# Optimization experiments

Measured on AMD Instinct MI355X. Metric: run time of the kernel, lower is better.

The kernel has to match this reference:

```python
import jax, jax.numpy as jnp
import numpy as np

B, C, H, K = 1024, 1000, 768, 128

def setup_inputs() -> dict:
    key = jax.random.key(0)
    k1, k2, k3, k4 = jax.random.split(key, 4)
    x = jax.random.normal(k1, (B, H), dtype=jnp.float32)
    y = jax.random.randint(k2, (B,), 0, C)
    class_weights = jax.random.normal(k3, (C, H, K), dtype=jnp.float32) * 0.1
    class_bias = jnp.zeros((C, H), dtype=jnp.float32)
    # torch.nn.Linear default init (uniform in +/- 1/sqrt(H))
    bound = 1.0 / np.sqrt(H)
    W_lin = jax.random.uniform(k4, (H, H), dtype=jnp.float32, minval=-bound, maxval=bound)
    b_lin = jnp.zeros((H,), dtype=jnp.float32)
    return {"x": x, "y": y, "class_weights": class_weights,
            "class_bias": class_bias, "W_lin": W_lin, "b_lin": b_lin}

def reference(x, y, class_weights, class_bias, W_lin, b_lin):
    # one-hot matmul gather == true indexed gather (same math)
    weights = class_weights[y]                # [B, H, K]
    neg_x = jax.nn.relu(-x)                   # [B, H]
    x1 = jnp.tanh(neg_x @ W_lin.T + b_lin)    # [B, H]
    # x1[B,1,H] @ weights[B,H,K] -> sum over singleton dim == [B, K]
    logits = jnp.einsum('bh,bhk->bk', x1, weights)
    return logits
```

## Files before the change

### kernel.cpp

```cpp
#include <hip/hip_runtime.h>
#include <hip/hip_bf16.h>
#include <cstddef>

#define B_SZ 1024
#define C_SZ 1000
#define H_SZ 768
#define K_SZ 128

typedef __attribute__((ext_vector_type(8))) short bf16x8;
typedef __attribute__((ext_vector_type(4))) float f32x4;

#define WS_NEGX_OFF 0
#define WS_W_OFF    1572864
#define WS_X1_OFF   4194304

__global__ __launch_bounds__(256) void convert_pack(
    const float* __restrict__ x, const float* __restrict__ W,
    ushort* __restrict__ negx, ushort* __restrict__ Wb)
{
    const int NX = B_SZ * H_SZ / 4;
    const int NW = H_SZ * H_SZ / 4;
    int i = blockIdx.x * 256 + threadIdx.x;
    if (i < NX) {
        float4 v = ((const float4*)x)[i];
        union { ushort u[4]; ushort4 v4; } o;
        o.u[0] = __bfloat16_as_ushort(__float2bfloat16(fmaxf(-v.x, 0.f)));
        o.u[1] = __bfloat16_as_ushort(__float2bfloat16(fmaxf(-v.y, 0.f)));
        o.u[2] = __bfloat16_as_ushort(__float2bfloat16(fmaxf(-v.z, 0.f)));
        o.u[3] = __bfloat16_as_ushort(__float2bfloat16(fmaxf(-v.w, 0.f)));
        ((ushort4*)negx)[i] = o.v4;
    } else {
        int j = i - NX;
        if (j < NW) {
            float4 v = ((const float4*)W)[j];
            union { ushort u[4]; ushort4 v4; } o;
            o.u[0] = __bfloat16_as_ushort(__float2bfloat16(v.x));
            o.u[1] = __bfloat16_as_ushort(__float2bfloat16(v.y));
            o.u[2] = __bfloat16_as_ushort(__float2bfloat16(v.z));
            o.u[3] = __bfloat16_as_ushort(__float2bfloat16(v.w));
            ((ushort4*)Wb)[j] = o.v4;
        }
    }
}

__global__ __launch_bounds__(256) void mfma_gemm_tanh(
    const ushort* __restrict__ A, const ushort* __restrict__ Bw,
    const float* __restrict__ bias, float* __restrict__ x1)
{
    const int LDA = 40;
    __shared__ ushort sA[64 * LDA];
    __shared__ ushort sB[64 * LDA];

    const int t    = threadIdx.x;
    const int wave = t >> 6;
    const int lane = t & 63;
    const int wm   = wave >> 1;
    const int wn   = wave & 1;
    const int m0   = blockIdx.y * 64;
    const int n0   = blockIdx.x * 64;

    const int lr = t >> 2;
    const int lc = (t & 3) * 8;

    f32x4 acc[2][2] = {};

    const int fr = lane & 15;
    const int fk = (lane >> 4) * 8;

    for (int k0 = 0; k0 < H_SZ; k0 += 32) {
        *(bf16x8*)(&sA[lr * LDA + lc]) =
            *(const bf16x8*)(&A[(size_t)(m0 + lr) * H_SZ + k0 + lc]);
        *(bf16x8*)(&sB[lr * LDA + lc]) =
            *(const bf16x8*)(&Bw[(size_t)(n0 + lr) * H_SZ + k0 + lc]);
        __syncthreads();

        #pragma unroll
        for (int fi = 0; fi < 2; ++fi) {
            bf16x8 af = *(const bf16x8*)(&sA[(wm * 32 + fi * 16 + fr) * LDA + fk]);
            #pragma unroll
            for (int fj = 0; fj < 2; ++fj) {
                bf16x8 bf = *(const bf16x8*)(&sB[(wn * 32 + fj * 16 + fr) * LDA + fk]);
                acc[fi][fj] = __builtin_amdgcn_mfma_f32_16x16x32_bf16(
                    af, bf, acc[fi][fj], 0, 0, 0);
            }
        }
        __syncthreads();
    }

    const int col   = lane & 15;
    const int rbase = (lane >> 4) * 4;
    #pragma unroll
    for (int fi = 0; fi < 2; ++fi) {
        #pragma unroll
        for (int fj = 0; fj < 2; ++fj) {
            const int n  = n0 + wn * 32 + fj * 16 + col;
            const float bv = bias[n];
            #pragma unroll
            for (int r = 0; r < 4; ++r) {
                const int m = m0 + wm * 32 + fi * 16 + rbase + r;
                x1[(size_t)m * H_SZ + n] = tanhf(acc[fi][fj][r] + bv);
            }
        }
    }
}

__global__ __launch_bounds__(256) void gather_dot(
    const float* __restrict__ x1, const int* __restrict__ y,
    const float* __restrict__ cw, float* __restrict__ out)
{
    const int b   = blockIdx.x;
    const int t   = threadIdx.x;
    const int k4  = t & 31;
    const int hg  = t >> 5;

    __shared__ float sx[H_SZ];
    __shared__ float4 red[256];

    const int cls = y[b];
    const float4* __restrict__ wrow =
        (const float4*)(cw + (size_t)cls * H_SZ * K_SZ);

    for (int i = t; i < H_SZ; i += 256)
        sx[i] = x1[(size_t)b * H_SZ + i];
    __syncthreads();

    float4 acc = {0.f, 0.f, 0.f, 0.f};
    #pragma unroll 4
    for (int h = hg; h < H_SZ; h += 8) {
        const float  xv = sx[h];
        const float4 w  = wrow[h * 32 + k4];
        acc.x += xv * w.x;
        acc.y += xv * w.y;
        acc.z += xv * w.z;
        acc.w += xv * w.w;
    }

    red[t] = acc;
    __syncthreads();
    if (t < 128) {
        float4 o = red[t + 128];
        red[t].x += o.x; red[t].y += o.y; red[t].z += o.z; red[t].w += o.w;
    }
    __syncthreads();
    if (t < 64) {
        float4 o = red[t + 64];
        red[t].x += o.x; red[t].y += o.y; red[t].z += o.z; red[t].w += o.w;
    }
    __syncthreads();
    if (t < 32) {
        float4 r = red[t];
        float4 o = red[t + 32];
        r.x += o.x; r.y += o.y; r.z += o.z; r.w += o.w;
        ((float4*)out)[(size_t)b * 32 + t] = r;
    }
}

extern "C" void kernel_launch(void* const* d_in, const int* in_sizes, int n_in,
                              void* d_out, int out_size, void* d_ws, size_t ws_size,
                              hipStream_t stream) {
    const float* x    = (const float*)d_in[0];
    const int*   y    = (const int*)  d_in[1];
    const float* cw   = (const float*)d_in[2];
    const float* Wlin = (const float*)d_in[4];
    const float* blin = (const float*)d_in[5];
    float* out = (float*)d_out;

    char* ws = (char*)d_ws;
    ushort* negx = (ushort*)(ws + WS_NEGX_OFF);
    ushort* Wb   = (ushort*)(ws + WS_W_OFF);
    float*  x1   = (float*) (ws + WS_X1_OFF);

    const int total4 = (B_SZ * H_SZ + H_SZ * H_SZ) / 4;
    convert_pack<<<(total4 + 255) / 256, 256, 0, stream>>>(x, Wlin, negx, Wb);

    dim3 g1(H_SZ / 64, B_SZ / 64);
    mfma_gemm_tanh<<<g1, 256, 0, stream>>>(negx, Wb, blin, x1);

    gather_dot<<<B_SZ, 256, 0, stream>>>(x1, y, cw, out);
}
```

Before: 513.8 us.

## Fuse relu/bf16 conversion into GEMM load path with register prefetch

Removes the separate convert_pack kernel. The GEMM now loads fp32 x and W directly, applies relu(-x) and converts to bf16 in registers before writing to shared memory. It also prefetches the next K-slice into registers while the MFMAs for the current slice run. The gather_dot kernel gets a vectorized x1 load, deeper unrolling and a single-step 8-way reduction in place of the tree, cutting kernel launches and barriers. In exchange, each GEMM block converts data redundantly across tiles and reads twice as many global bytes per element.

```diff
diff --git a/kernel.cpp b/kernel.cpp
--- a/kernel.cpp
+++ b/kernel.cpp
@@ -10,41 +10,13 @@
 typedef __attribute__((ext_vector_type(8))) short bf16x8;
 typedef __attribute__((ext_vector_type(4))) float f32x4;
 
-#define WS_NEGX_OFF 0
-#define WS_W_OFF    1572864
-#define WS_X1_OFF   4194304
 
-__global__ __launch_bounds__(256) void convert_pack(
-    const float* __restrict__ x, const float* __restrict__ W,
-    ushort* __restrict__ negx, ushort* __restrict__ Wb)
-{
-    const int NX = B_SZ * H_SZ / 4;
-    const int NW = H_SZ * H_SZ / 4;
-    int i = blockIdx.x * 256 + threadIdx.x;
-    if (i < NX) {
-        float4 v = ((const float4*)x)[i];
-        union { ushort u[4]; ushort4 v4; } o;
-        o.u[0] = __bfloat16_as_ushort(__float2bfloat16(fmaxf(-v.x, 0.f)));
-        o.u[1] = __bfloat16_as_ushort(__float2bfloat16(fmaxf(-v.y, 0.f)));
-        o.u[2] = __bfloat16_as_ushort(__float2bfloat16(fmaxf(-v.z, 0.f)));
-        o.u[3] = __bfloat16_as_ushort(__float2bfloat16(fmaxf(-v.w, 0.f)));
-        ((ushort4*)negx)[i] = o.v4;
-    } else {
-        int j = i - NX;
-        if (j < NW) {
-            float4 v = ((const float4*)W)[j];
-            union { ushort u[4]; ushort4 v4; } o;
-            o.u[0] = __bfloat16_as_ushort(__float2bfloat16(v.x));
-            o.u[1] = __bfloat16_as_ushort(__float2bfloat16(v.y));
-            o.u[2] = __bfloat16_as_ushort(__float2bfloat16(v.z));
-            o.u[3] = __bfloat16_as_ushort(__float2bfloat16(v.w));
-            ((ushort4*)Wb)[j] = o.v4;
-        }
-    }
+__device__ __forceinline__ ushort bfc(float f) {
+    return __bfloat16_as_ushort(__float2bfloat16(f));
 }
 
 __global__ __launch_bounds__(256) void mfma_gemm_tanh(
-    const ushort* __restrict__ A, const ushort* __restrict__ Bw,
+    const float* __restrict__ X, const float* __restrict__ W,
     const float* __restrict__ bias, float* __restrict__ x1)
 {
     const int LDA = 40;
@@ -62,17 +34,41 @@
     const int lr = t >> 2;
     const int lc = (t & 3) * 8;
 
+    const float* __restrict__ xrow = X + (size_t)(m0 + lr) * H_SZ + lc;
+    const float* __restrict__ wrow = W + (size_t)(n0 + lr) * H_SZ + lc;
+    ushort* sa = &sA[lr * LDA + lc];
+    ushort* sb = &sB[lr * LDA + lc];
+
     f32x4 acc[2][2] = {};
 
     const int fr = lane & 15;
     const int fk = (lane >> 4) * 8;
 
+    float4 a0 = *(const float4*)(xrow);
+    float4 a1 = *(const float4*)(xrow + 4);
+    float4 b0 = *(const float4*)(wrow);
+    float4 b1 = *(const float4*)(wrow + 4);
+
     for (int k0 = 0; k0 < H_SZ; k0 += 32) {
-        *(bf16x8*)(&sA[lr * LDA + lc]) =
-            *(const bf16x8*)(&A[(size_t)(m0 + lr) * H_SZ + k0 + lc]);
-        *(bf16x8*)(&sB[lr * LDA + lc]) =
-            *(const bf16x8*)(&Bw[(size_t)(n0 + lr) * H_SZ + k0 + lc]);
+        union { ushort u[8]; bf16x8 v; } pa, pb;
+        pa.u[0] = bfc(fmaxf(-a0.x, 0.f)); pa.u[1] = bfc(fmaxf(-a0.y, 0.f));
+        pa.u[2] = bfc(fmaxf(-a0.z, 0.f)); pa.u[3] = bfc(fmaxf(-a0.w, 0.f));
+        pa.u[4] = bfc(fmaxf(-a1.x, 0.f)); pa.u[5] = bfc(fmaxf(-a1.y, 0.f));
+        pa.u[6] = bfc(fmaxf(-a1.z, 0.f)); pa.u[7] = bfc(fmaxf(-a1.w, 0.f));
+        pb.u[0] = bfc(b0.x); pb.u[1] = bfc(b0.y);
+        pb.u[2] = bfc(b0.z); pb.u[3] = bfc(b0.w);
+        pb.u[4] = bfc(b1.x); pb.u[5] = bfc(b1.y);
+        pb.u[6] = bfc(b1.z); pb.u[7] = bfc(b1.w);
+        *(bf16x8*)sa = pa.v;
+        *(bf16x8*)sb = pb.v;
         __syncthreads();
+
+        if (k0 + 32 < H_SZ) {
+            a0 = *(const float4*)(xrow + k0 + 32);
+            a1 = *(const float4*)(xrow + k0 + 36);
+            b0 = *(const float4*)(wrow + k0 + 32);
+            b1 = *(const float4*)(wrow + k0 + 36);
+        }
 
         #pragma unroll
         for (int fi = 0; fi < 2; ++fi) {
@@ -108,50 +104,36 @@
     const float* __restrict__ x1, const int* __restrict__ y,
     const float* __restrict__ cw, float* __restrict__ out)
 {
-    const int b   = blockIdx.x;
-    const int t   = threadIdx.x;
-    const int k4  = t & 31;
-    const int hg  = t >> 5;
+    const int b  = blockIdx.x;
+    const int t  = threadIdx.x;
+    const int k4 = t & 31;
+    const int hg = t >> 5;
 
     __shared__ float sx[H_SZ];
-    __shared__ float4 red[256];
+    __shared__ f32x4 red[256];
 
     const int cls = y[b];
-    const float4* __restrict__ wrow =
-        (const float4*)(cw + (size_t)cls * H_SZ * K_SZ);
+    const f32x4* __restrict__ wrow =
+        (const f32x4*)(cw + (size_t)cls * H_SZ * K_SZ);
 
-    for (int i = t; i < H_SZ; i += 256)
-        sx[i] = x1[(size_t)b * H_SZ + i];
+    if (t < H_SZ / 4)
+        ((f32x4*)sx)[t] = ((const f32x4*)(x1 + (size_t)b * H_SZ))[t];
     __syncthreads();
 
-    float4 acc = {0.f, 0.f, 0.f, 0.f};
-    #pragma unroll 4
+    f32x4 acc = {};
+    #pragma unroll 8
     for (int h = hg; h < H_SZ; h += 8) {
-        const float  xv = sx[h];
-        const float4 w  = wrow[h * 32 + k4];
-        acc.x += xv * w.x;
-        acc.y += xv * w.y;
-        acc.z += xv * w.z;
-        acc.w += xv * w.w;
+        acc += wrow[h * 32 + k4] * sx[h];
     }
 
     red[t] = acc;
     __syncthreads();
-    if (t < 128) {
-        float4 o = red[t + 128];
-        red[t].x += o.x; red[t].y += o.y; red[t].z += o.z; red[t].w += o.w;
-    }
-    __syncthreads();
-    if (t < 64) {
-        float4 o = red[t + 64];
-        red[t].x += o.x; red[t].y += o.y; red[t].z += o.z; red[t].w += o.w;
-    }
-    __syncthreads();
     if (t < 32) {
-        float4 r = red[t];
-        float4 o = red[t + 32];
-        r.x += o.x; r.y += o.y; r.z += o.z; r.w += o.w;
-        ((float4*)out)[(size_t)b * 32 + t] = r;
+        f32x4 r = red[t];
+        #pragma unroll
+        for (int j = 1; j < 8; ++j)
+            r += red[t + 32 * j];
+        ((f32x4*)out)[(size_t)b * 32 + t] = r;
     }
 }
 
@@ -165,16 +147,10 @@
     const float* blin = (const float*)d_in[5];
     float* out = (float*)d_out;
 
-    char* ws = (char*)d_ws;
-    ushort* negx = (ushort*)(ws + WS_NEGX_OFF);
-    ushort* Wb   = (ushort*)(ws + WS_W_OFF);
-    float*  x1   = (float*) (ws + WS_X1_OFF);
-
-    const int total4 = (B_SZ * H_SZ + H_SZ * H_SZ) / 4;
-    convert_pack<<<(total4 + 255) / 256, 256, 0, stream>>>(x, Wlin, negx, Wb);
+    float* x1 = (float*)d_ws;
 
     dim3 g1(H_SZ / 64, B_SZ / 64);
-    mfma_gemm_tanh<<<g1, 256, 0, stream>>>(negx, Wb, blin, x1);
+    mfma_gemm_tanh<<<g1, 256, 0, stream>>>(x, Wlin, blin, x1);
 
     gather_dot<<<B_SZ, 256, 0, stream>>>(x1, y, cw, out);
 }
```

After: 518.7 us. No clear change (+1.0%).
